# Kernel optimization log

Measured on AMD Instinct MI355X. Metric: run time of the kernel, lower is better.

## Reference

```python
import jax, jax.numpy as jnp
import numpy as np

TEMP = 0.1      # temperature
REG = 0.1       # ot_reg
MAX_ITER = 100  # Sinkhorn-style scaling iterations (original early-stops on tol; fixed-point is identical post-convergence)

B, D, N_PER = 64, 128, 512  # examples, embed dim, nodes/tokens per example


def _normalize(x):
    # torch F.normalize(dim=1): x / max(||x||, eps)
    n = jnp.linalg.norm(x, axis=1, keepdims=True)
    return x / jnp.maximum(n, 1e-12)


def setup_inputs() -> dict:
    key = jax.random.key(0)
    k0, k1, k2, k3 = jax.random.split(key, 4)
    N = B * N_PER
    return {
        "struct_global": jax.random.normal(k0, (B, D), jnp.float32),
        "seq_global": jax.random.normal(k1, (B, D), jnp.float32),
        "struct_nodes": jax.random.normal(k2, (N, D), jnp.float32),
        "seq_tokens": jax.random.normal(k3, (N, D), jnp.float32),
        # sorted, equal-size segments: example i owns rows [i*N_PER, (i+1)*N_PER)
        "batch_idx": jnp.repeat(jnp.arange(B), N_PER),
    }


def _global_nt_xent(struct_emb, seq_emb):
    s = _normalize(struct_emb)
    q = _normalize(seq_emb)
    sim = (s @ q.T) / TEMP                      # [B, B]
    loss_i = -jnp.mean(jnp.diagonal(jax.nn.log_softmax(sim, axis=1)))
    loss_j = -jnp.mean(jnp.diagonal(jax.nn.log_softmax(sim.T, axis=1)))
    return (loss_i + loss_j) / 2.0


def _local_ot_loss(struct_nodes, seq_tokens):
    # batch_idx is sorted equal-size segments -> dense batched reshape
    sn = _normalize(struct_nodes).reshape(B, N_PER, D)
    st = _normalize(seq_tokens).reshape(B, N_PER, D)
    C = -jnp.einsum('bnd,bmd->bnm', sn, st)     # [B, n, m] cost
    n = m = N_PER
    # Original detaches cost to numpy before OT -> transport plan P is a constant w.r.t. grads
    C_sg = jax.lax.stop_gradient(C)
    P0 = jnp.exp(-C_sg / REG)
    a = jnp.full((B, n), 1.0 / n, C.dtype)
    b = jnp.full((B, m), 1.0 / m, C.dtype)

    def body(_, uv):
        u, v = uv
        # Jacobi-style update: both use the previous (u, v), matching the source
        u_new = a / jnp.einsum('bnm,bm->bn', P0, v)
        v_new = b / jnp.einsum('bnm,bn->bm', P0, u)
        u_new = jnp.nan_to_num(u_new, nan=1.0 / n, posinf=1.0 / n, neginf=1.0 / n)
        v_new = jnp.nan_to_num(v_new, nan=1.0 / m, posinf=1.0 / m, neginf=1.0 / m)
        return (u_new, v_new)

    u, v = jax.lax.fori_loop(0, MAX_ITER, body, (a, b))  # init u=1/n, v=1/m as in source
    P = u[:, :, None] * P0 * v[:, None, :]      # diag(u) @ P0 @ diag(v)
    total = jnp.sum(P * C)                      # grads flow through C only
    return total / B


def reference(struct_global, seq_global, struct_nodes, seq_tokens, batch_idx):
    global_loss = _global_nt_xent(struct_global, seq_global)
    local_loss = _local_ot_loss(struct_nodes, seq_tokens)
    total_loss = global_loss + local_loss
    return (global_loss, local_loss, total_loss)
```

## Files before the change

### kernel.cpp

```cpp
#include <hip/hip_runtime.h>
#include <cstdint>
#include <cmath>

#define NB_EX 64
#define DIMD 128
#define NP 512
#define NITER 100
constexpr float MARG = 1.0f / 512.0f;

__device__ __forceinline__ float bf2f_lo(unsigned w) { return __uint_as_float(w << 16); }
__device__ __forceinline__ float bf2f_hi(unsigned w) { return __uint_as_float(w & 0xFFFF0000u); }
__device__ __forceinline__ unsigned short f2bf(float f) {
    unsigned u = __float_as_uint(f);
    u += 0x7FFFu + ((u >> 16) & 1u);
    return (unsigned short)(u >> 16);
}
__device__ __forceinline__ float wred64(float v) {
#pragma unroll
    for (int m = 1; m < 64; m <<= 1) v += __shfl_xor(v, m, 64);
    return v;
}

__device__ __forceinline__ int self_detect(const unsigned* probe, int t) {
    __shared__ int sd_cnt[4];
    unsigned w = probe[t];
    unsigned e = (w >> 7) & 0xFFu;
    unsigned long long m = __ballot(e >= 110u && e <= 130u);
    if ((t & 63) == 0) sd_cnt[t >> 6] = __popcll(m);
    __syncthreads();
    int c = sd_cnt[0] + sd_cnt[1] + sd_cnt[2] + sd_cnt[3];
    __syncthreads();
    return c >= 128;
}

#define O_SIMG   0
#define O_RNAN   16384
#define O_RNBN   147456
#define O_COLP   278528
#define O_P0     4472832
#define COLP_BANK (64 * 8 * 512)

__global__ void k_rnormAB(const void* anr, const void* bnr, float* rnan, float* rnbn) {
    int t = threadIdx.x;
    int flag = self_detect((const unsigned*)anr, t);
    int gr  = blockIdx.x * 4 + (t >> 6);
    int lane = t & 63;
    const void* in = (gr < 32768) ? anr : bnr;
    float* rn      = (gr < 32768) ? rnan : rnbn;
    int row = gr & 32767;
    float f0, f1;
    if (flag) {
        unsigned w = ((const unsigned*)in)[row * 64 + lane];
        f0 = bf2f_lo(w); f1 = bf2f_hi(w);
    } else {
        float2 v = ((const float2*)in)[row * 64 + lane];
        f0 = v.x; f1 = v.y;
    }
    float ss = wred64(f0 * f0 + f1 * f1);
    if (lane == 0) rn[row] = 1.0f / fmaxf(sqrtf(ss), 1e-12f);
}

__global__ void k_simg(const void* sgr, const void* qgr, float* simg) {
    __shared__ float rls[128];
    int t = threadIdx.x;
    int flag = self_detect((const unsigned*)sgr, t);
    int w = t >> 6, lane = t & 63;
    for (int rr = 0; rr < 32; rr++) {
        int ri = w * 32 + rr;
        const void* base = (ri < 64) ? sgr : qgr;
        int row = ri & 63;
        float f0, f1;
        if (flag) {
            unsigned wd = ((const unsigned*)base)[row * 64 + lane];
            f0 = bf2f_lo(wd); f1 = bf2f_hi(wd);
        } else {
            float2 v = ((const float2*)base)[row * 64 + lane];
            f0 = v.x; f1 = v.y;
        }
        float ss = wred64(f0 * f0 + f1 * f1);
        if (lane == 0) rls[ri] = 1.0f / fmaxf(sqrtf(ss), 1e-12f);
    }
    __syncthreads();
    int g = blockIdx.x * 256 + t;
    int i = g >> 6, j = g & 63;
    float dot = 0.f;
    if (flag) {
        const unsigned* a = (const unsigned*)sgr + i * 64;
        const unsigned* b = (const unsigned*)qgr + j * 64;
        for (int k = 0; k < 64; k++) {
            unsigned wa = a[k], wb = b[k];
            dot += bf2f_lo(wa) * bf2f_lo(wb);
            dot += bf2f_hi(wa) * bf2f_hi(wb);
        }
    } else {
        const float4* a = (const float4*)sgr + i * 32;
        const float4* b = (const float4*)qgr + j * 32;
        for (int k = 0; k < 32; k++) {
            float4 x = a[k], y = b[k];
            dot += x.x * y.x + x.y * y.y + x.z * y.z + x.w * y.w;
        }
    }
    simg[g] = dot * rls[i] * rls[64 + j] * 10.0f;
}

__global__ void k_gloss(const float* __restrict__ simg, float* outf) {
    __shared__ float red[64];
    int i = threadIdx.x;
    if (i < 64) {
        float m = -1e30f;
        for (int j = 0; j < 64; j++) m = fmaxf(m, simg[i * 64 + j]);
        float se = 0.f;
        for (int j = 0; j < 64; j++) se += expf(simg[i * 64 + j] - m);
        float rl = simg[i * 64 + i] - (m + logf(se));
        float m2 = -1e30f;
        for (int j = 0; j < 64; j++) m2 = fmaxf(m2, simg[j * 64 + i]);
        float se2 = 0.f;
        for (int j = 0; j < 64; j++) se2 += expf(simg[j * 64 + i] - m2);
        float cl = simg[i * 64 + i] - (m2 + logf(se2));
        red[i] = rl + cl;
    }
    __syncthreads();
    if (i == 0) {
        float s = 0.f;
        for (int k = 0; k < 64; k++) s += red[k];
        float g = -s / 128.0f;
        outf[0] = g;
        outf[1] = 0.0f;
        outf[2] = g;
    }
}

__global__ void k_build(const void* anr, const void* bnr, const float* rnan, const float* rnbn,
                        unsigned short* p0) {
    int t  = threadIdx.x;
    int flag = self_detect((const unsigned*)anr, t);
    int b   = blockIdx.y;
    int r0t = (blockIdx.x >> 2) * 128;
    int c0t = (blockIdx.x & 3) * 128;
    __shared__ float As[128][33];
    __shared__ float Bs[128][33];
    int tr = t >> 4, tc = t & 15;
    float acc[8][8];
#pragma unroll
    for (int i = 0; i < 8; i++)
#pragma unroll
        for (int j = 0; j < 8; j++) acc[i][j] = 0.f;

    for (int kc = 0; kc < 4; kc++) {
        for (int ii = 0; ii < 4; ii++) {
            int idx = t + 256 * ii;
            int r = idx >> 3, c4 = idx & 7;
            {
                int grow = b * NP + r0t + r;
                float sc = rnan[grow];
                float f0, f1, f2, f3;
                if (flag) {
                    const unsigned* src = (const unsigned*)anr + ((grow * DIMD + kc * 32 + c4 * 4) >> 1);
                    unsigned w0 = src[0], w1 = src[1];
                    f0 = bf2f_lo(w0); f1 = bf2f_hi(w0); f2 = bf2f_lo(w1); f3 = bf2f_hi(w1);
                } else {
                    float4 v = *((const float4*)((const float*)anr + grow * DIMD + kc * 32 + c4 * 4));
                    f0 = v.x; f1 = v.y; f2 = v.z; f3 = v.w;
                }
                As[r][c4 * 4 + 0] = f0 * sc; As[r][c4 * 4 + 1] = f1 * sc;
                As[r][c4 * 4 + 2] = f2 * sc; As[r][c4 * 4 + 3] = f3 * sc;
            }
            {
                int grow = b * NP + c0t + r;
                float sc = rnbn[grow];
                float f0, f1, f2, f3;
                if (flag) {
                    const unsigned* src = (const unsigned*)bnr + ((grow * DIMD + kc * 32 + c4 * 4) >> 1);
                    unsigned w0 = src[0], w1 = src[1];
                    f0 = bf2f_lo(w0); f1 = bf2f_hi(w0); f2 = bf2f_lo(w1); f3 = bf2f_hi(w1);
                } else {
                    float4 v = *((const float4*)((const float*)bnr + grow * DIMD + kc * 32 + c4 * 4));
                    f0 = v.x; f1 = v.y; f2 = v.z; f3 = v.w;
                }
                Bs[r][c4 * 4 + 0] = f0 * sc; Bs[r][c4 * 4 + 1] = f1 * sc;
                Bs[r][c4 * 4 + 2] = f2 * sc; Bs[r][c4 * 4 + 3] = f3 * sc;
            }
        }
        __syncthreads();
        for (int kk = 0; kk < 32; kk++) {
            float av[8], bv[8];
#pragma unroll
            for (int i = 0; i < 8; i++) av[i] = As[tr * 8 + i][kk];
#pragma unroll
            for (int j = 0; j < 8; j++) bv[j] = Bs[tc * 8 + j][kk];
#pragma unroll
            for (int i = 0; i < 8; i++)
#pragma unroll
                for (int j = 0; j < 8; j++) acc[i][j] += av[i] * bv[j];
        }
        __syncthreads();
    }
#pragma unroll
    for (int i = 0; i < 8; i++) {
        int grow = b * NP + r0t + tr * 8 + i;
        unsigned short h[8];
#pragma unroll
        for (int j = 0; j < 8; j++) h[j] = f2bf(expf(acc[i][j] * 10.0f));
        uint4 pk;
        pk.x = (unsigned)h[0] | ((unsigned)h[1] << 16);
        pk.y = (unsigned)h[2] | ((unsigned)h[3] << 16);
        pk.z = (unsigned)h[4] | ((unsigned)h[5] << 16);
        pk.w = (unsigned)h[6] | ((unsigned)h[7] << 16);
        *((uint4*)(p0 + ((size_t)grow * NP + c0t + tc * 8))) = pk;
    }
}

__global__ __launch_bounds__(256, 2) void k_persist(const unsigned short* __restrict__ p0,
                                                    unsigned* __restrict__ colp,
                                                    float* __restrict__ outf) {
    int blk = blockIdx.x;
    int rb  = blk >> 6;
    int b   = blk & 63;
    int rowbase = rb * 64;
    int t = threadIdx.x, w = t >> 6, lane = t & 63;

    __shared__ float colred[4][512];
    __shared__ float v_s[512];
    __shared__ float bs[4];

    uint4 pw[16];
#pragma unroll
    for (int r = 0; r < 16; r++) {
        int row = rowbase + w * 16 + r;
        pw[r] = ((const uint4*)(p0 + (((size_t)(b << 9) + row) << 9)))[lane];
    }
    float u_loc[16];
#pragma unroll
    for (int r = 0; r < 16; r++) u_loc[r] = MARG;

    int col0 = t, col1 = t + 256;

#pragma unroll 1
    for (int it = 0; it < NITER; ++it) {
        float ca[8];
#pragma unroll
        for (int k = 0; k < 8; ++k) ca[k] = 0.f;
#pragma unroll
        for (int r = 0; r < 16; ++r) {
            float u_r = u_loc[r];
            uint4 pv = pw[r];
            ca[0] += bf2f_lo(pv.x) * u_r; ca[1] += bf2f_hi(pv.x) * u_r;
            ca[2] += bf2f_lo(pv.y) * u_r; ca[3] += bf2f_hi(pv.y) * u_r;
            ca[4] += bf2f_lo(pv.z) * u_r; ca[5] += bf2f_hi(pv.z) * u_r;
            ca[6] += bf2f_lo(pv.w) * u_r; ca[7] += bf2f_hi(pv.w) * u_r;
        }
#pragma unroll
        for (int k = 0; k < 8; ++k) colred[w][lane * 8 + k] = ca[k];
        __syncthreads();
        unsigned tag_w = (unsigned)(it + 1);
        {
            float s0 = colred[0][col0] + colred[1][col0] + colred[2][col0] + colred[3][col0];
            float s1 = colred[0][col1] + colred[1][col1] + colred[2][col1] + colred[3][col1];
            unsigned p0w = ((unsigned)f2bf(s0) << 16) | tag_w;
            unsigned p1w = ((unsigned)f2bf(s1) << 16) | tag_w;
            unsigned* cw = colp + (((((it + 1) & 3) * 64 + b) * 8 + rb) << 9);
            __hip_atomic_store(&cw[col0], p0w, __ATOMIC_RELAXED, __HIP_MEMORY_SCOPE_AGENT);
            __hip_atomic_store(&cw[col1], p1w, __ATOMIC_RELAXED, __HIP_MEMORY_SCOPE_AGENT);
        }
        if (it == 0) {
            v_s[col0] = MARG;
            v_s[col1] = MARG;
        } else {
            unsigned tag = (unsigned)it;
            const unsigned* crd = colp + ((((it & 3) * 64 + b) * 8) << 9);
            unsigned got0[8], got1[8];
            for (;;) {
                bool o = true;
#pragma unroll
                for (int p = 0; p < 8; p++) {
                    got0[p] = __hip_atomic_load(&crd[(p << 9) + col0], __ATOMIC_RELAXED,
                                                __HIP_MEMORY_SCOPE_AGENT);
                    got1[p] = __hip_atomic_load(&crd[(p << 9) + col1], __ATOMIC_RELAXED,
                                                __HIP_MEMORY_SCOPE_AGENT);
                }
#pragma unroll
                for (int p = 0; p < 8; p++)
                    o = o && ((got0[p] & 0xFFFFu) == tag) && ((got1[p] & 0xFFFFu) == tag);
                if (o) break;
                __builtin_amdgcn_s_sleep(1);
            }
            float r0 = 0.f, r1 = 0.f;
#pragma unroll
            for (int p = 0; p < 8; p++) {
                r0 += __uint_as_float(got0[p] & 0xFFFF0000u);
                r1 += __uint_as_float(got1[p] & 0xFFFF0000u);
            }
            float q0 = MARG / r0; if (!isfinite(q0)) q0 = MARG;
            float q1 = MARG / r1; if (!isfinite(q1)) q1 = MARG;
            v_s[col0] = q0;
            v_s[col1] = q1;
        }
        __syncthreads();
        float vr[8];
#pragma unroll
        for (int k = 0; k < 8; ++k) vr[k] = v_s[lane * 8 + k];
#pragma unroll
        for (int r = 0; r < 16; ++r) {
            uint4 pv = pw[r];
            float rd = bf2f_lo(pv.x) * vr[0] + bf2f_hi(pv.x) * vr[1]
                     + bf2f_lo(pv.y) * vr[2] + bf2f_hi(pv.y) * vr[3]
                     + bf2f_lo(pv.z) * vr[4] + bf2f_hi(pv.z) * vr[5]
                     + bf2f_lo(pv.w) * vr[6] + bf2f_hi(pv.w) * vr[7];
            rd = wred64(rd);
            float qq = MARG / rd;
            if (!isfinite(qq)) qq = MARG;
            u_loc[r] = qq;
        }
    }

    {
        unsigned tag = 100u;
        const unsigned* crd = colp + (((0 * 64 + b) * 8) << 9);
        unsigned got0[8], got1[8];
        for (;;) {
            bool o = true;
#pragma unroll
            for (int p = 0; p < 8; p++) {
                got0[p] = __hip_atomic_load(&crd[(p << 9) + col0], __ATOMIC_RELAXED,
                                            __HIP_MEMORY_SCOPE_AGENT);
                got1[p] = __hip_atomic_load(&crd[(p << 9) + col1], __ATOMIC_RELAXED,
                                            __HIP_MEMORY_SCOPE_AGENT);
            }
#pragma unroll
            for (int p = 0; p < 8; p++)
                o = o && ((got0[p] & 0xFFFFu) == tag) && ((got1[p] & 0xFFFFu) == tag);
            if (o) break;
            __builtin_amdgcn_s_sleep(1);
        }
        float r0 = 0.f, r1 = 0.f;
#pragma unroll
        for (int p = 0; p < 8; p++) {
            r0 += __uint_as_float(got0[p] & 0xFFFF0000u);
            r1 += __uint_as_float(got1[p] & 0xFFFF0000u);
        }
        float q0 = MARG / r0; if (!isfinite(q0)) q0 = MARG;
        float q1 = MARG / r1; if (!isfinite(q1)) q1 = MARG;
        v_s[col0] = q0;
        v_s[col1] = q1;
    }
    __syncthreads();
    float vr[8];
#pragma unroll
    for (int k = 0; k < 8; ++k) vr[k] = v_s[lane * 8 + k];
    float acc = 0.f;
#pragma unroll
    for (int r = 0; r < 16; ++r) {
        float u_r = u_loc[r];
        uint4 pv = pw[r];
        float f[8];
        f[0] = bf2f_lo(pv.x); f[1] = bf2f_hi(pv.x);
        f[2] = bf2f_lo(pv.y); f[3] = bf2f_hi(pv.y);
        f[4] = bf2f_lo(pv.z); f[5] = bf2f_hi(pv.z);
        f[6] = bf2f_lo(pv.w); f[7] = bf2f_hi(pv.w);
#pragma unroll
        for (int k = 0; k < 8; ++k) {
            float p = f[k];
            acc += u_r * p * vr[k] * (-0.1f) * logf(p);
        }
    }
    acc = wred64(acc);
    if (lane == 0) bs[w] = acc;
    __syncthreads();
    if (t == 0) {
        float c = (bs[0] + bs[1] + bs[2] + bs[3]) * (1.0f / 64.0f);
        atomicAdd(&outf[1], c);
        atomicAdd(&outf[2], c);
    }
}

extern "C" void kernel_launch(void* const* d_in, const int* in_sizes, int n_in,
                              void* d_out, int out_size, void* d_ws, size_t ws_size,
                              hipStream_t stream) {
    const void* sg = d_in[0];
    const void* qg = d_in[1];
    const void* an = d_in[2];
    const void* bn = d_in[3];
    char* ws = (char*)d_ws;
    float* outf = (float*)d_out;

    float* simg     = (float*)(ws + O_SIMG);
    float* rnan     = (float*)(ws + O_RNAN);
    float* rnbn     = (float*)(ws + O_RNBN);
    unsigned* colp  = (unsigned*)(ws + O_COLP);
    unsigned short* p0 = (unsigned short*)(ws + O_P0);

    k_rnormAB<<<16384, 256, 0, stream>>>(an, bn, rnan, rnbn);
    k_simg<<<16, 256, 0, stream>>>(sg, qg, simg);
    k_gloss<<<1, 256, 0, stream>>>(simg, outf);
    k_build<<<dim3(16, 64), 256, 0, stream>>>(an, bn, rnan, rnbn, p0);
    k_persist<<<512, 256, 0, stream>>>(p0, colp, outf);
}
```

Baseline: 760.8 us.

## Interleave the two independent Jacobi Sinkhorn chains to overlap cross-block exchanges

The Jacobi-style Sinkhorn update makes u depend only on the previous v and v only on the previous u, so the sequence splits into two independent chains. The persistent kernel now advances both chains in one loop of 50 steps. While one chain's column partial sums are being published to and polled from global memory by the other row-blocks, the kernel computes the other chain's row scaling and column partials. This is meant to hide the inter-block spin-wait latency that used to serialize every iteration. In exchange it needs more shared memory and registers (separate reduction buffers and u arrays), four colp banks with a new tag scheme, and more complex bookkeeping of which chain supplies the final u and v.

```diff
diff --git a/kernel.cpp b/kernel.cpp
--- a/kernel.cpp
+++ b/kernel.cpp
@@ -5,7 +5,6 @@
 #define NB_EX 64
 #define DIMD 128
 #define NP 512
-#define NITER 100
 constexpr float MARG = 1.0f / 512.0f;
 
 __device__ __forceinline__ float bf2f_lo(unsigned w) { return __uint_as_float(w << 16); }
@@ -38,7 +37,6 @@
 #define O_RNBN   147456
 #define O_COLP   278528
 #define O_P0     4472832
-#define COLP_BANK (64 * 8 * 512)
 
 __global__ void k_rnormAB(const void* anr, const void* bnr, float* rnan, float* rnbn) {
     int t = threadIdx.x;
@@ -219,8 +217,10 @@
     int rowbase = rb * 64;
     int t = threadIdx.x, w = t >> 6, lane = t & 63;
 
-    __shared__ float colred[4][512];
-    __shared__ float v_s[512];
+    __shared__ float credU[4][512];
+    __shared__ float credV[4][512];
+    __shared__ float v_sU[512];
+    __shared__ float v_sV[512];
     __shared__ float bs[4];
 
     uint4 pw[16];
@@ -229,45 +229,79 @@
         int row = rowbase + w * 16 + r;
         pw[r] = ((const uint4*)(p0 + (((size_t)(b << 9) + row) << 9)))[lane];
     }
-    float u_loc[16];
-#pragma unroll
-    for (int r = 0; r < 16; r++) u_loc[r] = MARG;
-
+    float uU[16], uV[16];
+#pragma unroll
+    for (int r = 0; r < 16; r++) uU[r] = MARG;
     int col0 = t, col1 = t + 256;
+    v_sV[col0] = MARG; v_sV[col1] = MARG;
+    __syncthreads();
 
 #pragma unroll 1
-    for (int it = 0; it < NITER; ++it) {
-        float ca[8];
-#pragma unroll
-        for (int k = 0; k < 8; ++k) ca[k] = 0.f;
-#pragma unroll
-        for (int r = 0; r < 16; ++r) {
-            float u_r = u_loc[r];
-            uint4 pv = pw[r];
-            ca[0] += bf2f_lo(pv.x) * u_r; ca[1] += bf2f_hi(pv.x) * u_r;
-            ca[2] += bf2f_lo(pv.y) * u_r; ca[3] += bf2f_hi(pv.y) * u_r;
-            ca[4] += bf2f_lo(pv.z) * u_r; ca[5] += bf2f_hi(pv.z) * u_r;
-            ca[6] += bf2f_lo(pv.w) * u_r; ca[7] += bf2f_hi(pv.w) * u_r;
-        }
-#pragma unroll
-        for (int k = 0; k < 8; ++k) colred[w][lane * 8 + k] = ca[k];
-        __syncthreads();
-        unsigned tag_w = (unsigned)(it + 1);
-        {
-            float s0 = colred[0][col0] + colred[1][col0] + colred[2][col0] + colred[3][col0];
-            float s1 = colred[0][col1] + colred[1][col1] + colred[2][col1] + colred[3][col1];
-            unsigned p0w = ((unsigned)f2bf(s0) << 16) | tag_w;
-            unsigned p1w = ((unsigned)f2bf(s1) << 16) | tag_w;
-            unsigned* cw = colp + (((((it + 1) & 3) * 64 + b) * 8 + rb) << 9);
-            __hip_atomic_store(&cw[col0], p0w, __ATOMIC_RELAXED, __HIP_MEMORY_SCOPE_AGENT);
-            __hip_atomic_store(&cw[col1], p1w, __ATOMIC_RELAXED, __HIP_MEMORY_SCOPE_AGENT);
-        }
-        if (it == 0) {
-            v_s[col0] = MARG;
-            v_s[col1] = MARG;
-        } else {
-            unsigned tag = (unsigned)it;
-            const unsigned* crd = colp + ((((it & 3) * 64 + b) * 8) << 9);
+    for (int s = 0; s < 50; ++s) {
+        unsigned tag = (unsigned)(s + 1);
+        int bank = s & 1;
+        {
+            float ca[8];
+#pragma unroll
+            for (int k = 0; k < 8; ++k) ca[k] = 0.f;
+#pragma unroll
+            for (int r = 0; r < 16; ++r) {
+                float u_r = uU[r];
+                uint4 pv = pw[r];
+                ca[0] += bf2f_lo(pv.x) * u_r; ca[1] += bf2f_hi(pv.x) * u_r;
+                ca[2] += bf2f_lo(pv.y) * u_r; ca[3] += bf2f_hi(pv.y) * u_r;
+                ca[4] += bf2f_lo(pv.z) * u_r; ca[5] += bf2f_hi(pv.z) * u_r;
+                ca[6] += bf2f_lo(pv.w) * u_r; ca[7] += bf2f_hi(pv.w) * u_r;
+            }
+#pragma unroll
+            for (int k = 0; k < 8; ++k) credU[w][lane * 8 + k] = ca[k];
+        }
+        __syncthreads();
+        {
+            float s0 = credU[0][col0] + credU[1][col0] + credU[2][col0] + credU[3][col0];
+            float s1 = credU[0][col1] + credU[1][col1] + credU[2][col1] + credU[3][col1];
+            unsigned pk0 = ((unsigned)f2bf(s0) << 16) | tag;
+            unsigned pk1 = ((unsigned)f2bf(s1) << 16) | tag;
+            unsigned* cw = colp + ((((bank * 64 + b) * 8 + rb) << 9));
+            __hip_atomic_store(&cw[col0], pk0, __ATOMIC_RELAXED, __HIP_MEMORY_SCOPE_AGENT);
+            __hip_atomic_store(&cw[col1], pk1, __ATOMIC_RELAXED, __HIP_MEMORY_SCOPE_AGENT);
+        }
+        {
+            float vr[8];
+#pragma unroll
+            for (int k = 0; k < 8; ++k) vr[k] = v_sV[lane * 8 + k];
+#pragma unroll
+            for (int r = 0; r < 16; ++r) {
+                uint4 pv = pw[r];
+                float rd = bf2f_lo(pv.x) * vr[0] + bf2f_hi(pv.x) * vr[1]
+                         + bf2f_lo(pv.y) * vr[2] + bf2f_hi(pv.y) * vr[3]
+                         + bf2f_lo(pv.z) * vr[4] + bf2f_hi(pv.z) * vr[5]
+                         + bf2f_lo(pv.w) * vr[6] + bf2f_hi(pv.w) * vr[7];
+                rd = wred64(rd);
+                float q = MARG / rd;
+                if (!isfinite(q)) q = MARG;
+                uV[r] = q;
+            }
+        }
+        {
+            float ca[8];
+#pragma unroll
+            for (int k = 0; k < 8; ++k) ca[k] = 0.f;
+#pragma unroll
+            for (int r = 0; r < 16; ++r) {
+                float u_r = uV[r];
+                uint4 pv = pw[r];
+                ca[0] += bf2f_lo(pv.x) * u_r; ca[1] += bf2f_hi(pv.x) * u_r;
+                ca[2] += bf2f_lo(pv.y) * u_r; ca[3] += bf2f_hi(pv.y) * u_r;
+                ca[4] += bf2f_lo(pv.z) * u_r; ca[5] += bf2f_hi(pv.z) * u_r;
+                ca[6] += bf2f_lo(pv.w) * u_r; ca[7] += bf2f_hi(pv.w) * u_r;
+            }
+#pragma unroll
+            for (int k = 0; k < 8; ++k) credV[w][lane * 8 + k] = ca[k];
+        }
+        __syncthreads();
+        {
+            const unsigned* crd = colp + (((bank * 64 + b) * 8) << 9);
             unsigned got0[8], got1[8];
             for (;;) {
                 bool o = true;
@@ -292,65 +326,75 @@
             }
             float q0 = MARG / r0; if (!isfinite(q0)) q0 = MARG;
             float q1 = MARG / r1; if (!isfinite(q1)) q1 = MARG;
-            v_s[col0] = q0;
-            v_s[col1] = q1;
-        }
-        __syncthreads();
-        float vr[8];
-#pragma unroll
-        for (int k = 0; k < 8; ++k) vr[k] = v_s[lane * 8 + k];
-#pragma unroll
-        for (int r = 0; r < 16; ++r) {
-            uint4 pv = pw[r];
-            float rd = bf2f_lo(pv.x) * vr[0] + bf2f_hi(pv.x) * vr[1]
-                     + bf2f_lo(pv.y) * vr[2] + bf2f_hi(pv.y) * vr[3]
-                     + bf2f_lo(pv.z) * vr[4] + bf2f_hi(pv.z) * vr[5]
-                     + bf2f_lo(pv.w) * vr[6] + bf2f_hi(pv.w) * vr[7];
-            rd = wred64(rd);
-            float qq = MARG / rd;
-            if (!isfinite(qq)) qq = MARG;
-            u_loc[r] = qq;
-        }
-    }
-
-    {
-        unsigned tag = 100u;
-        const unsigned* crd = colp + (((0 * 64 + b) * 8) << 9);
-        unsigned got0[8], got1[8];
-        for (;;) {
-            bool o = true;
+            v_sU[col0] = q0;
+            v_sU[col1] = q1;
+        }
+        __syncthreads();
+        {
+            float s0 = credV[0][col0] + credV[1][col0] + credV[2][col0] + credV[3][col0];
+            float s1 = credV[0][col1] + credV[1][col1] + credV[2][col1] + credV[3][col1];
+            unsigned pk0 = ((unsigned)f2bf(s0) << 16) | tag;
+            unsigned pk1 = ((unsigned)f2bf(s1) << 16) | tag;
+            unsigned* cw = colp + (((((2 + bank) * 64 + b) * 8 + rb) << 9));
+            __hip_atomic_store(&cw[col0], pk0, __ATOMIC_RELAXED, __HIP_MEMORY_SCOPE_AGENT);
+            __hip_atomic_store(&cw[col1], pk1, __ATOMIC_RELAXED, __HIP_MEMORY_SCOPE_AGENT);
+        }
+        {
+            float vr[8];
+#pragma unroll
+            for (int k = 0; k < 8; ++k) vr[k] = v_sU[lane * 8 + k];
+#pragma unroll
+            for (int r = 0; r < 16; ++r) {
+                uint4 pv = pw[r];
+                float rd = bf2f_lo(pv.x) * vr[0] + bf2f_hi(pv.x) * vr[1]
+                         + bf2f_lo(pv.y) * vr[2] + bf2f_hi(pv.y) * vr[3]
+                         + bf2f_lo(pv.z) * vr[4] + bf2f_hi(pv.z) * vr[5]
+                         + bf2f_lo(pv.w) * vr[6] + bf2f_hi(pv.w) * vr[7];
+                rd = wred64(rd);
+                float q = MARG / rd;
+                if (!isfinite(q)) q = MARG;
+                uU[r] = q;
+            }
+        }
+        {
+            const unsigned* crd = colp + ((((2 + bank) * 64 + b) * 8) << 9);
+            unsigned got0[8], got1[8];
+            for (;;) {
+                bool o = true;
+#pragma unroll
+                for (int p = 0; p < 8; p++) {
+                    got0[p] = __hip_atomic_load(&crd[(p << 9) + col0], __ATOMIC_RELAXED,
+                                                __HIP_MEMORY_SCOPE_AGENT);
+                    got1[p] = __hip_atomic_load(&crd[(p << 9) + col1], __ATOMIC_RELAXED,
+                                                __HIP_MEMORY_SCOPE_AGENT);
+                }
+#pragma unroll
+                for (int p = 0; p < 8; p++)
+                    o = o && ((got0[p] & 0xFFFFu) == tag) && ((got1[p] & 0xFFFFu) == tag);
+                if (o) break;
+                __builtin_amdgcn_s_sleep(1);
+            }
+            float r0 = 0.f, r1 = 0.f;
 #pragma unroll
             for (int p = 0; p < 8; p++) {
-                got0[p] = __hip_atomic_load(&crd[(p << 9) + col0], __ATOMIC_RELAXED,
-                                            __HIP_MEMORY_SCOPE_AGENT);
-                got1[p] = __hip_atomic_load(&crd[(p << 9) + col1], __ATOMIC_RELAXED,
-                                            __HIP_MEMORY_SCOPE_AGENT);
-            }
-#pragma unroll
-            for (int p = 0; p < 8; p++)
-                o = o && ((got0[p] & 0xFFFFu) == tag) && ((got1[p] & 0xFFFFu) == tag);
-            if (o) break;
-            __builtin_amdgcn_s_sleep(1);
-        }
-        float r0 = 0.f, r1 = 0.f;
-#pragma unroll
-        for (int p = 0; p < 8; p++) {
-            r0 += __uint_as_float(got0[p] & 0xFFFF0000u);
-            r1 += __uint_as_float(got1[p] & 0xFFFF0000u);
-        }
-        float q0 = MARG / r0; if (!isfinite(q0)) q0 = MARG;
-        float q1 = MARG / r1; if (!isfinite(q1)) q1 = MARG;
-        v_s[col0] = q0;
-        v_s[col1] = q1;
-    }
-    __syncthreads();
+                r0 += __uint_as_float(got0[p] & 0xFFFF0000u);
+                r1 += __uint_as_float(got1[p] & 0xFFFF0000u);
+            }
+            float q0 = MARG / r0; if (!isfinite(q0)) q0 = MARG;
+            float q1 = MARG / r1; if (!isfinite(q1)) q1 = MARG;
+            v_sV[col0] = q0;
+            v_sV[col1] = q1;
+        }
+        __syncthreads();
+    }
+
     float vr[8];
 #pragma unroll
-    for (int k = 0; k < 8; ++k) vr[k] = v_s[lane * 8 + k];
+    for (int k = 0; k < 8; ++k) vr[k] = v_sV[lane * 8 + k];
     float acc = 0.f;
 #pragma unroll
     for (int r = 0; r < 16; ++r) {
-        float u_r = u_loc[r];
+        float u_r = uU[r];
         uint4 pv = pw[r];
         float f[8];
         f[0] = bf2f_lo(pv.x); f[1] = bf2f_hi(pv.x);
```

Measured after the change: 1.530 ms. +101.1%, slower.
